# Optimization experiments

Measured on AMD Instinct MI355X. Metric: run time of the kernel, lower is better.

The kernel has to match this reference:

```python
import jax, jax.numpy as jnp
import numpy as np

B, C_IN, L = 256, 4, 2048
HNODE, GLEN = 256, 24
SIGMA_CONV, SIGMA_NEU = 0.1, 0.1
DROPPROB = 0.5


def setup_inputs() -> dict:
    key = jax.random.key(0)
    ks = jax.random.split(key, 7)
    x = jax.random.normal(ks[0], (B, C_IN, L), dtype=jnp.float32)
    wConv = SIGMA_CONV * jax.random.normal(ks[1], (HNODE, C_IN, GLEN), dtype=jnp.float32)
    wRect = -jax.random.normal(ks[2], (HNODE,), dtype=jnp.float32)
    wHidden = 0.3 * jax.random.normal(ks[3], (2 * HNODE, 2 * HNODE), dtype=jnp.float32)
    wHiddenBias = 0.3 * jax.random.normal(ks[4], (2 * HNODE,), dtype=jnp.float32)
    wNeu = SIGMA_NEU * jax.random.normal(ks[5], (2 * HNODE, 1), dtype=jnp.float32)
    wNeuBias = SIGMA_NEU * jax.random.normal(ks[6], (1,), dtype=jnp.float32)
    return {"x": x, "wConv": wConv, "wRect": wRect, "wHidden": wHidden,
            "wHiddenBias": wHiddenBias, "wNeu": wNeu, "wNeuBias": wNeuBias}


def reference(x, wConv, wRect, wHidden, wHiddenBias, wNeu, wNeuBias):
    # conv1d, stride 1, no padding: [B, HNODE, L-GLEN+1]
    conv = jax.lax.conv_general_dilated(
        x, wConv, window_strides=(1,), padding='VALID',
        dimension_numbers=('NCH', 'OIH', 'NCH'))
    rect = jnp.maximum(conv + wRect[None, :, None], 0.0)  # bias + relu-clamp
    maxPool = jnp.max(rect, axis=2)   # [B, HNODE]
    avgPool = jnp.mean(rect, axis=2)  # [B, HNODE]
    pool = jnp.concatenate([maxPool, avgPool], axis=1)  # [B, 2*HNODE]
    hid = jnp.maximum(pool @ wHidden + wHiddenBias, 0.0)
    out = DROPPROB * (hid @ wNeu) + wNeuBias  # [B, 1]
    return out
```

## Files before the change

kernel.cpp:

```cpp
#include <hip/hip_runtime.h>
#include <stdint.h>

#define CIN   4
#define LEN   2048
#define HN    256
#define GL    24
#define LOUT  2025
#define XP    2080

typedef short  s16x8 __attribute__((ext_vector_type(8)));
typedef float  f32x4 __attribute__((ext_vector_type(4)));

static __device__ __forceinline__ uint16_t f2bf(float f) {
    union { float f; uint32_t u; } v; v.f = f;
    uint32_t u = v.u;
    return (uint16_t)((u + 0x7FFFu + ((u >> 16) & 1u)) >> 16);
}

#define MKFRAG(dd, p) \
    ({ uint32_t f0_, f1_, f2_, f3_; \
       if (((p) & 1) == 0) { \
           f0_ = dd[(p)/2];   f1_ = dd[(p)/2+1]; \
           f2_ = dd[(p)/2+2]; f3_ = dd[(p)/2+3]; \
       } else { \
           f0_ = __builtin_amdgcn_alignbit(dd[((p)+1)/2],   dd[((p)-1)/2],   16); \
           f1_ = __builtin_amdgcn_alignbit(dd[((p)+1)/2+1], dd[((p)-1)/2+1], 16); \
           f2_ = __builtin_amdgcn_alignbit(dd[((p)+1)/2+2], dd[((p)-1)/2+2], 16); \
           f3_ = __builtin_amdgcn_alignbit(dd[((p)+1)/2+3], dd[((p)-1)/2+3], 16); \
       } \
       uint4 fu_ = {f0_, f1_, f2_, f3_}; __builtin_bit_cast(s16x8, fu_); })

__global__ __launch_bounds__(1024, 4) void conv_pool_kernel(
    const float* __restrict__ x, const float* __restrict__ wConv,
    const float* __restrict__ wRect, float* __restrict__ pool)
{
    __shared__ uint16_t xs[CIN * XP];
    __shared__ float pmax_l[2][HN];
    __shared__ float psum_l[2][HN];

    const int tid  = threadIdx.x;
    const int b    = blockIdx.x;
    const int lane = tid & 63;
    const int wid  = tid >> 6;
    const int wp   = wid & 7;
    const int wh   = wid >> 3;
    const int n    = lane & 15;
    const int q    = lane >> 4;

    const float* xb = x + (size_t)b * (CIN * LEN);
    #pragma unroll
    for (int it = 0; it < 2; ++it) {
        int i = (tid + it * 1024) * 4;
        float4 v = *(const float4*)(xb + i);
        int c = i >> 11, off = i & 2047;
        uint64_t pk =  (uint64_t)f2bf(v.x)
                    | ((uint64_t)f2bf(v.y) << 16)
                    | ((uint64_t)f2bf(v.z) << 32)
                    | ((uint64_t)f2bf(v.w) << 48);
        *(uint64_t*)&xs[c * XP + off] = pk;
    }
    if (tid < 64) {
        int c = tid >> 4, o = (tid & 15) * 2;
        *(uint32_t*)&xs[c * XP + 2048 + o] = 0u;
    }

    s16x8 bfrag[2][3];
    float negb[2];
    #pragma unroll
    for (int s = 0; s < 2; ++s) {
        int h = wp * 32 + s * 16 + n;
        negb[s] = -wRect[h];
        #pragma unroll
        for (int ks = 0; ks < 3; ++ks) {
            int jb = ks * 4 + q;
            const float* wp_ = wConv + h * (CIN * GL) + jb * 8;
            float4 w0 = *(const float4*)(wp_);
            float4 w1 = *(const float4*)(wp_ + 4);
            s16x8 f;
            f[0]=(short)f2bf(w0.x); f[1]=(short)f2bf(w0.y);
            f[2]=(short)f2bf(w0.z); f[3]=(short)f2bf(w0.w);
            f[4]=(short)f2bf(w1.x); f[5]=(short)f2bf(w1.y);
            f[6]=(short)f2bf(w1.z); f[7]=(short)f2bf(w1.w);
            bfrag[s][ks] = f;
        }
    }

    int abase[3];
    #pragma unroll
    for (int ks = 0; ks < 3; ++ks) {
        int jb = ks * 4 + q;
        int c = jb / 3, g0 = (jb % 3) * 8;
        abase[ks] = c * XP + g0 + 8 * n;
    }

    __syncthreads();

    float rawmax[2] = {-1e30f, -1e30f};
    float sums[2]   = {0.f, 0.f};
    const f32x4 fzero = {0.f, 0.f, 0.f, 0.f};

    #pragma unroll 1
    for (int jj = 0; jj < 8; ++jj) {
        const int j = wh * 8 + jj;
        const bool tail = (j == 15);

        uint32_t d0[8], d1[8], d2[8];
        {
            const uint4 r0 = *(const uint4*)&xs[abase[0] + 128 * j];
            const uint4 r1 = *(const uint4*)&xs[abase[0] + 128 * j + 8];
            d0[0]=r0.x; d0[1]=r0.y; d0[2]=r0.z; d0[3]=r0.w;
            d0[4]=r1.x; d0[5]=r1.y; d0[6]=r1.z; d0[7]=r1.w;
        }
        {
            const uint4 r0 = *(const uint4*)&xs[abase[1] + 128 * j];
            const uint4 r1 = *(const uint4*)&xs[abase[1] + 128 * j + 8];
            d1[0]=r0.x; d1[1]=r0.y; d1[2]=r0.z; d1[3]=r0.w;
            d1[4]=r1.x; d1[5]=r1.y; d1[6]=r1.z; d1[7]=r1.w;
        }
        {
            const uint4 r0 = *(const uint4*)&xs[abase[2] + 128 * j];
            const uint4 r1 = *(const uint4*)&xs[abase[2] + 128 * j + 8];
            d2[0]=r0.x; d2[1]=r0.y; d2[2]=r0.z; d2[3]=r0.w;
            d2[4]=r1.x; d2[5]=r1.y; d2[6]=r1.z; d2[7]=r1.w;
        }

        #pragma unroll
        for (int p = 0; p < 8; ++p) {
            s16x8 a0 = MKFRAG(d0, p);
            s16x8 a1 = MKFRAG(d1, p);
            s16x8 a2 = MKFRAG(d2, p);
            f32x4 acc[2];
            acc[0] = __builtin_amdgcn_mfma_f32_16x16x32_bf16(a0, bfrag[0][0], fzero, 0, 0, 0);
            acc[1] = __builtin_amdgcn_mfma_f32_16x16x32_bf16(a0, bfrag[1][0], fzero, 0, 0, 0);
            acc[0] = __builtin_amdgcn_mfma_f32_16x16x32_bf16(a1, bfrag[0][1], acc[0], 0, 0, 0);
            acc[1] = __builtin_amdgcn_mfma_f32_16x16x32_bf16(a1, bfrag[1][1], acc[1], 0, 0, 0);
            acc[0] = __builtin_amdgcn_mfma_f32_16x16x32_bf16(a2, bfrag[0][2], acc[0], 0, 0, 0);
            acc[1] = __builtin_amdgcn_mfma_f32_16x16x32_bf16(a2, bfrag[1][2], acc[1], 0, 0, 0);

            if (!tail) {
                #pragma unroll
                for (int s = 0; s < 2; ++s) {
                    const f32x4 a = acc[s];
                    float t0 = fmaxf(a[0], negb[s]), t1 = fmaxf(a[1], negb[s]);
                    float t2 = fmaxf(a[2], negb[s]), t3 = fmaxf(a[3], negb[s]);
                    sums[s] += (t0 + t1) + (t2 + t3);
                    rawmax[s] = fmaxf(fmaxf(rawmax[s], a[0]), a[1]);
                    rawmax[s] = fmaxf(fmaxf(rawmax[s], a[2]), a[3]);
                }
            } else {
                #pragma unroll
                for (int s = 0; s < 2; ++s) {
                    const f32x4 a = acc[s];
                    #pragma unroll
                    for (int r = 0; r < 4; ++r) {
                        int tpos = p + 128 * 15 + 32 * q + 8 * r;
                        float t = (tpos < LOUT) ? fmaxf(a[r], negb[s])
                                                : negb[s];
                        sums[s]   += t;
                        rawmax[s]  = fmaxf(rawmax[s], t);
                    }
                }
            }
        }
    }

    #pragma unroll
    for (int s = 0; s < 2; ++s) {
        float m  = rawmax[s], sm = sums[s];
        m  = fmaxf(m, __shfl_xor(m, 16, 64));  sm += __shfl_xor(sm, 16, 64);
        m  = fmaxf(m, __shfl_xor(m, 32, 64));  sm += __shfl_xor(sm, 32, 64);
        if (q == 0) {
            int h = wp * 32 + s * 16 + n;
            pmax_l[wh][h] = m;
            psum_l[wh][h] = sm;
        }
    }
    __syncthreads();

    if (tid < HN) {
        float m   = fmaxf(pmax_l[0][tid], pmax_l[1][tid]);
        float sm  = psum_l[0][tid] + psum_l[1][tid];
        float bia = wRect[tid];
        pool[(size_t)b * 512 + tid]       = fmaxf(m + bia, 0.f);
        pool[(size_t)b * 512 + 256 + tid] = (sm + 2048.f * bia) * (1.0f / 2025.0f);
    }
}

__global__ __launch_bounds__(256, 4) void mlp_kernel(
    const float* __restrict__ pool, const float* __restrict__ wH,
    const float* __restrict__ bH, const float* __restrict__ wNeu,
    const float* __restrict__ wNeuB, float* __restrict__ out)
{
    __shared__ float pl[8][512];

    const int tid = threadIdx.x;
    const int og  = blockIdx.x & 7;
    const int bg  = blockIdx.x >> 3;
    const int o   = og * 64 + (tid & 63);
    const int wv  = tid >> 6;

    const float* ps = pool + (size_t)bg * 8 * 512;
    #pragma unroll
    for (int it = 0; it < 4; ++it) {
        int i = (tid + it * 256) * 4;
        *(float4*)&pl[0][i] = *(const float4*)(ps + i);
    }
    __syncthreads();

    float acc0 = 0.f, acc1 = 0.f;
    const float* prow0 = &pl[wv * 2][0];
    const float* prow1 = &pl[wv * 2 + 1][0];
    #pragma unroll 4
    for (int i = 0; i < 512; i += 4) {
        float4 p0 = *(const float4*)(prow0 + i);
        float4 p1 = *(const float4*)(prow1 + i);
        float w0 = wH[(i + 0) * 512 + o];
        float w1 = wH[(i + 1) * 512 + o];
        float w2 = wH[(i + 2) * 512 + o];
        float w3 = wH[(i + 3) * 512 + o];
        acc0 = fmaf(p0.x, w0, acc0); acc0 = fmaf(p0.y, w1, acc0);
        acc0 = fmaf(p0.z, w2, acc0); acc0 = fmaf(p0.w, w3, acc0);
        acc1 = fmaf(p1.x, w0, acc1); acc1 = fmaf(p1.y, w1, acc1);
        acc1 = fmaf(p1.z, w2, acc1); acc1 = fmaf(p1.w, w3, acc1);
    }
    float hb  = bH[o];
    float wn  = wNeu[o];
    float v0  = fmaxf(acc0 + hb, 0.f) * wn;
    float v1  = fmaxf(acc1 + hb, 0.f) * wn;
    #pragma unroll
    for (int dlt = 1; dlt < 64; dlt <<= 1) {
        v0 += __shfl_xor(v0, dlt, 64);
        v1 += __shfl_xor(v1, dlt, 64);
    }
    if ((tid & 63) == 0) {
        int b0 = bg * 8 + wv * 2;
        float bias = (og == 0) ? wNeuB[0] : 0.f;
        atomicAdd(&out[b0],     0.5f * v0 + bias);
        atomicAdd(&out[b0 + 1], 0.5f * v1 + bias);
    }
}

extern "C" void kernel_launch(void* const* d_in, const int* in_sizes, int n_in,
                              void* d_out, int out_size, void* d_ws, size_t ws_size,
                              hipStream_t stream) {
    const float* x        = (const float*)d_in[0];
    const float* wConv    = (const float*)d_in[1];
    const float* wRect    = (const float*)d_in[2];
    const float* wHidden  = (const float*)d_in[3];
    const float* wHidBias = (const float*)d_in[4];
    const float* wNeu     = (const float*)d_in[5];
    const float* wNeuBias = (const float*)d_in[6];
    float* out  = (float*)d_out;
    float* pool = (float*)d_ws;

    hipMemsetAsync(d_out, 0, 256 * sizeof(float), stream);
    conv_pool_kernel<<<256, 1024, 0, stream>>>(x, wConv, wRect, pool);
    mlp_kernel<<<256, 256, 0, stream>>>(pool, wHidden, wHidBias, wNeu, wNeuBias, out);
}
```

Baseline: 125.4 us.

## Split conv over two blocks per sample and merge pool partials in MLP

Each sample's sequence is now split across two blocks of the conv kernel, giving 512 blocks in place of 256 so all compute units get work. Each block loads only its half of the input plus a halo, with smaller shared memory. Partial max and sum values go to a global buffer, and the bias, relu and mean finalisation moves into the MLP kernel's load phase. This adds duplicated weight-fragment setup and halo loads per block, plus an extra partial-buffer read in the MLP.

```diff
diff --git a/kernel.cpp b/kernel.cpp
--- a/kernel.cpp
+++ b/kernel.cpp
@@ -6,10 +6,12 @@
 #define HN    256
 #define GL    24
 #define LOUT  2025
-#define XP    2080
+#define XPH   1056
 
 typedef short  s16x8 __attribute__((ext_vector_type(8)));
 typedef float  f32x4 __attribute__((ext_vector_type(4)));
+
+__device__ float g_part[256][2][512];
 
 static __device__ __forceinline__ uint16_t f2bf(float f) {
     union { float f; uint32_t u; } v; v.f = f;
@@ -30,38 +32,38 @@
        } \
        uint4 fu_ = {f0_, f1_, f2_, f3_}; __builtin_bit_cast(s16x8, fu_); })
 
-__global__ __launch_bounds__(1024, 4) void conv_pool_kernel(
+__global__ __launch_bounds__(1024, 8) void conv_pool_kernel(
     const float* __restrict__ x, const float* __restrict__ wConv,
-    const float* __restrict__ wRect, float* __restrict__ pool)
+    const float* __restrict__ wRect)
 {
-    __shared__ uint16_t xs[CIN * XP];
+    __shared__ uint16_t xs[CIN * XPH];
     __shared__ float pmax_l[2][HN];
     __shared__ float psum_l[2][HN];
 
     const int tid  = threadIdx.x;
-    const int b    = blockIdx.x;
+    const int b    = blockIdx.x >> 1;
+    const int wh   = blockIdx.x & 1;
     const int lane = tid & 63;
     const int wid  = tid >> 6;
     const int wp   = wid & 7;
-    const int wh   = wid >> 3;
+    const int wq   = wid >> 3;
     const int n    = lane & 15;
     const int q    = lane >> 4;
 
     const float* xb = x + (size_t)b * (CIN * LEN);
-    #pragma unroll
-    for (int it = 0; it < 2; ++it) {
-        int i = (tid + it * 1024) * 4;
-        float4 v = *(const float4*)(xb + i);
-        int c = i >> 11, off = i & 2047;
-        uint64_t pk =  (uint64_t)f2bf(v.x)
-                    | ((uint64_t)f2bf(v.y) << 16)
-                    | ((uint64_t)f2bf(v.z) << 32)
-                    | ((uint64_t)f2bf(v.w) << 48);
-        *(uint64_t*)&xs[c * XP + off] = pk;
-    }
-    if (tid < 64) {
-        int c = tid >> 4, o = (tid & 15) * 2;
-        *(uint32_t*)&xs[c * XP + 2048 + o] = 0u;
+    for (int f = tid; f < CIN * (XPH / 4); f += 1024) {
+        int c = f / (XPH / 4);
+        int k4 = (f - c * (XPH / 4)) * 4;
+        int p0 = wh * 1024 + k4;
+        uint64_t pk = 0;
+        if (p0 < LEN) {
+            float4 v = *(const float4*)(xb + c * LEN + p0);
+            pk =  (uint64_t)f2bf(v.x)
+               | ((uint64_t)f2bf(v.y) << 16)
+               | ((uint64_t)f2bf(v.z) << 32)
+               | ((uint64_t)f2bf(v.w) << 48);
+        }
+        *(uint64_t*)&xs[c * XPH + k4] = pk;
     }
 
     s16x8 bfrag[2][3];
@@ -90,7 +92,7 @@
     for (int ks = 0; ks < 3; ++ks) {
         int jb = ks * 4 + q;
         int c = jb / 3, g0 = (jb % 3) * 8;
-        abase[ks] = c * XP + g0 + 8 * n;
+        abase[ks] = c * XPH + g0 + 8 * n;
     }
 
     __syncthreads();
@@ -100,26 +102,26 @@
     const f32x4 fzero = {0.f, 0.f, 0.f, 0.f};
 
     #pragma unroll 1
-    for (int jj = 0; jj < 8; ++jj) {
-        const int j = wh * 8 + jj;
-        const bool tail = (j == 15);
+    for (int tt = 0; tt < 4; ++tt) {
+        const int jl = wq * 4 + tt;
+        const bool tail = (wh == 1) && (jl == 7);
 
         uint32_t d0[8], d1[8], d2[8];
         {
-            const uint4 r0 = *(const uint4*)&xs[abase[0] + 128 * j];
-            const uint4 r1 = *(const uint4*)&xs[abase[0] + 128 * j + 8];
+            const uint4 r0 = *(const uint4*)&xs[abase[0] + 128 * jl];
+            const uint4 r1 = *(const uint4*)&xs[abase[0] + 128 * jl + 8];
             d0[0]=r0.x; d0[1]=r0.y; d0[2]=r0.z; d0[3]=r0.w;
             d0[4]=r1.x; d0[5]=r1.y; d0[6]=r1.z; d0[7]=r1.w;
         }
         {
-            const uint4 r0 = *(const uint4*)&xs[abase[1] + 128 * j];
-            const uint4 r1 = *(const uint4*)&xs[abase[1] + 128 * j + 8];
+            const uint4 r0 = *(const uint4*)&xs[abase[1] + 128 * jl];
+            const uint4 r1 = *(const uint4*)&xs[abase[1] + 128 * jl + 8];
             d1[0]=r0.x; d1[1]=r0.y; d1[2]=r0.z; d1[3]=r0.w;
             d1[4]=r1.x; d1[5]=r1.y; d1[6]=r1.z; d1[7]=r1.w;
         }
         {
-            const uint4 r0 = *(const uint4*)&xs[abase[2] + 128 * j];
-            const uint4 r1 = *(const uint4*)&xs[abase[2] + 128 * j + 8];
+            const uint4 r0 = *(const uint4*)&xs[abase[2] + 128 * jl];
+            const uint4 r1 = *(const uint4*)&xs[abase[2] + 128 * jl + 8];
             d2[0]=r0.x; d2[1]=r0.y; d2[2]=r0.z; d2[3]=r0.w;
             d2[4]=r1.x; d2[5]=r1.y; d2[6]=r1.z; d2[7]=r1.w;
         }
@@ -171,23 +173,20 @@
         m  = fmaxf(m, __shfl_xor(m, 32, 64));  sm += __shfl_xor(sm, 32, 64);
         if (q == 0) {
             int h = wp * 32 + s * 16 + n;
-            pmax_l[wh][h] = m;
-            psum_l[wh][h] = sm;
+            pmax_l[wq][h] = m;
+            psum_l[wq][h] = sm;
         }
     }
     __syncthreads();
 
     if (tid < HN) {
-        float m   = fmaxf(pmax_l[0][tid], pmax_l[1][tid]);
-        float sm  = psum_l[0][tid] + psum_l[1][tid];
-        float bia = wRect[tid];
-        pool[(size_t)b * 512 + tid]       = fmaxf(m + bia, 0.f);
-        pool[(size_t)b * 512 + 256 + tid] = (sm + 2048.f * bia) * (1.0f / 2025.0f);
+        g_part[b][wh][tid]       = fmaxf(pmax_l[0][tid], pmax_l[1][tid]);
+        g_part[b][wh][256 + tid] = psum_l[0][tid] + psum_l[1][tid];
     }
 }
 
 __global__ __launch_bounds__(256, 4) void mlp_kernel(
-    const float* __restrict__ pool, const float* __restrict__ wH,
+    const float* __restrict__ wRect, const float* __restrict__ wH,
     const float* __restrict__ bH, const float* __restrict__ wNeu,
     const float* __restrict__ wNeuB, float* __restrict__ out)
 {
@@ -199,11 +198,30 @@
     const int o   = og * 64 + (tid & 63);
     const int wv  = tid >> 6;
 
-    const float* ps = pool + (size_t)bg * 8 * 512;
     #pragma unroll
     for (int it = 0; it < 4; ++it) {
-        int i = (tid + it * 256) * 4;
-        *(float4*)&pl[0][i] = *(const float4*)(ps + i);
+        int i   = (tid + it * 256) * 4;
+        int smp = i >> 9;
+        int c   = i & 511;
+        const float* p0 = &g_part[bg * 8 + smp][0][c];
+        const float* p1 = &g_part[bg * 8 + smp][1][c];
+        float4 v0 = *(const float4*)p0;
+        float4 v1 = *(const float4*)p1;
+        float4 r;
+        if (c < 256) {
+            float4 wr = *(const float4*)(wRect + c);
+            r.x = fmaxf(fmaxf(v0.x, v1.x) + wr.x, 0.f);
+            r.y = fmaxf(fmaxf(v0.y, v1.y) + wr.y, 0.f);
+            r.z = fmaxf(fmaxf(v0.z, v1.z) + wr.z, 0.f);
+            r.w = fmaxf(fmaxf(v0.w, v1.w) + wr.w, 0.f);
+        } else {
+            float4 wr = *(const float4*)(wRect + c - 256);
+            r.x = (v0.x + v1.x + 2048.f * wr.x) * (1.0f / 2025.0f);
+            r.y = (v0.y + v1.y + 2048.f * wr.y) * (1.0f / 2025.0f);
+            r.z = (v0.z + v1.z + 2048.f * wr.z) * (1.0f / 2025.0f);
+            r.w = (v0.w + v1.w + 2048.f * wr.w) * (1.0f / 2025.0f);
+        }
+        *(float4*)&pl[0][i] = r;
     }
     __syncthreads();
 
@@ -251,9 +269,9 @@
     const float* wNeu     = (const float*)d_in[5];
     const float* wNeuBias = (const float*)d_in[6];
     float* out  = (float*)d_out;
-    float* pool = (float*)d_ws;
+    (void)d_ws; (void)ws_size;
 
     hipMemsetAsync(d_out, 0, 256 * sizeof(float), stream);
-    conv_pool_kernel<<<256, 1024, 0, stream>>>(x, wConv, wRect, pool);
-    mlp_kernel<<<256, 256, 0, stream>>>(pool, wHidden, wHidBias, wNeu, wNeuBias, out);
-}
+    conv_pool_kernel<<<512, 1024, 0, stream>>>(x, wConv, wRect);
+    mlp_kernel<<<256, 256, 0, stream>>>(wRect, wHidden, wHidBias, wNeu, wNeuBias, out);
+}
```

New measurement: 338.3 us. 2.7x slower.

## Halve conv block size, widen per-wave channel tile, double-buffer LDS window loads

Applied to the files above, without the earlier changes.

The conv kernel moves from 1024 to 512 threads per block, and each wave now covers 64 output channels instead of 32. This lets every A fragment built from the input window feed four MFMA chains instead of two, so fewer LDS reads and alignbit fragment builds are needed per MFMA. The time loop is software-pipelined with two register buffers, so the next window's LDS load overlaps the current MFMA work. The pool workspace also moves to a device-global array. The cost is higher register pressure (twice the B fragments and accumulators), only 16 waves per block, and a waves_per_eu hint that limits occupancy.

```diff
diff --git a/kernel.cpp b/kernel.cpp
--- a/kernel.cpp
+++ b/kernel.cpp
@@ -10,6 +10,8 @@
 
 typedef short  s16x8 __attribute__((ext_vector_type(8)));
 typedef float  f32x4 __attribute__((ext_vector_type(4)));
+
+__device__ float g_pool[256 * 512];
 
 static __device__ __forceinline__ uint16_t f2bf(float f) {
     union { float f; uint32_t u; } v; v.f = f;
@@ -30,9 +32,71 @@
        } \
        uint4 fu_ = {f0_, f1_, f2_, f3_}; __builtin_bit_cast(s16x8, fu_); })
 
-__global__ __launch_bounds__(1024, 4) void conv_pool_kernel(
+static __device__ __forceinline__ void loadW(
+    uint32_t (&D)[3][8], const uint16_t* xs, const int (&abase)[3], int j)
+{
+    #pragma unroll
+    for (int ks = 0; ks < 3; ++ks) {
+        const uint4 r0 = *(const uint4*)&xs[abase[ks] + 128 * j];
+        const uint4 r1 = *(const uint4*)&xs[abase[ks] + 128 * j + 8];
+        D[ks][0] = r0.x; D[ks][1] = r0.y; D[ks][2] = r0.z; D[ks][3] = r0.w;
+        D[ks][4] = r1.x; D[ks][5] = r1.y; D[ks][6] = r1.z; D[ks][7] = r1.w;
+    }
+}
+
+static __device__ __forceinline__ void procW(
+    const uint32_t (&D)[3][8], const s16x8 (&bfrag)[4][3],
+    const float (&negb)[4], bool tail, int q,
+    float (&rawmax)[4], float (&sums)[4])
+{
+    const f32x4 fzero = {0.f, 0.f, 0.f, 0.f};
+    #pragma unroll
+    for (int p = 0; p < 8; ++p) {
+        s16x8 a0 = MKFRAG(D[0], p);
+        s16x8 a1 = MKFRAG(D[1], p);
+        s16x8 a2 = MKFRAG(D[2], p);
+        f32x4 acc[4];
+        #pragma unroll
+        for (int s = 0; s < 4; ++s)
+            acc[s] = __builtin_amdgcn_mfma_f32_16x16x32_bf16(a0, bfrag[s][0], fzero, 0, 0, 0);
+        #pragma unroll
+        for (int s = 0; s < 4; ++s)
+            acc[s] = __builtin_amdgcn_mfma_f32_16x16x32_bf16(a1, bfrag[s][1], acc[s], 0, 0, 0);
+        #pragma unroll
+        for (int s = 0; s < 4; ++s)
+            acc[s] = __builtin_amdgcn_mfma_f32_16x16x32_bf16(a2, bfrag[s][2], acc[s], 0, 0, 0);
+
+        if (!tail) {
+            #pragma unroll
+            for (int s = 0; s < 4; ++s) {
+                const f32x4 a = acc[s];
+                float t0 = fmaxf(a[0], negb[s]), t1 = fmaxf(a[1], negb[s]);
+                float t2 = fmaxf(a[2], negb[s]), t3 = fmaxf(a[3], negb[s]);
+                sums[s] += (t0 + t1) + (t2 + t3);
+                rawmax[s] = fmaxf(fmaxf(rawmax[s], a[0]), a[1]);
+                rawmax[s] = fmaxf(fmaxf(rawmax[s], a[2]), a[3]);
+            }
+        } else {
+            #pragma unroll
+            for (int s = 0; s < 4; ++s) {
+                const f32x4 a = acc[s];
+                #pragma unroll
+                for (int r = 0; r < 4; ++r) {
+                    int tpos = p + 128 * 15 + 32 * q + 8 * r;
+                    float t = (tpos < LOUT) ? fmaxf(a[r], negb[s])
+                                            : negb[s];
+                    sums[s]   += t;
+                    rawmax[s]  = fmaxf(rawmax[s], t);
+                }
+            }
+        }
+    }
+}
+
+__global__ __launch_bounds__(512) __attribute__((amdgpu_waves_per_eu(2, 2)))
+void conv_pool_kernel(
     const float* __restrict__ x, const float* __restrict__ wConv,
-    const float* __restrict__ wRect, float* __restrict__ pool)
+    const float* __restrict__ wRect)
 {
     __shared__ uint16_t xs[CIN * XP];
     __shared__ float pmax_l[2][HN];
@@ -42,15 +106,15 @@
     const int b    = blockIdx.x;
     const int lane = tid & 63;
     const int wid  = tid >> 6;
-    const int wp   = wid & 7;
-    const int wh   = wid >> 3;
+    const int ng   = wid & 3;
+    const int jh   = wid >> 2;
     const int n    = lane & 15;
     const int q    = lane >> 4;
 
     const float* xb = x + (size_t)b * (CIN * LEN);
     #pragma unroll
-    for (int it = 0; it < 2; ++it) {
-        int i = (tid + it * 1024) * 4;
+    for (int it = 0; it < 4; ++it) {
+        int i = (tid + it * 512) * 4;
         float4 v = *(const float4*)(xb + i);
         int c = i >> 11, off = i & 2047;
         uint64_t pk =  (uint64_t)f2bf(v.x)
@@ -64,11 +128,11 @@
         *(uint32_t*)&xs[c * XP + 2048 + o] = 0u;
     }
 
-    s16x8 bfrag[2][3];
-    float negb[2];
-    #pragma unroll
-    for (int s = 0; s < 2; ++s) {
-        int h = wp * 32 + s * 16 + n;
+    s16x8 bfrag[4][3];
+    float negb[4];
+    #pragma unroll
+    for (int s = 0; s < 4; ++s) {
+        int h = ng * 64 + s * 16 + n;
         negb[s] = -wRect[h];
         #pragma unroll
         for (int ks = 0; ks < 3; ++ks) {
@@ -95,84 +159,30 @@
 
     __syncthreads();
 
-    float rawmax[2] = {-1e30f, -1e30f};
-    float sums[2]   = {0.f, 0.f};
-    const f32x4 fzero = {0.f, 0.f, 0.f, 0.f};
-
+    float rawmax[4] = {-1e30f, -1e30f, -1e30f, -1e30f};
+    float sums[4]   = {0.f, 0.f, 0.f, 0.f};
+
+    const int j0 = jh * 8;
+    uint32_t dA[3][8], dB[3][8];
+    loadW(dA, xs, abase, j0);
     #pragma unroll 1
-    for (int jj = 0; jj < 8; ++jj) {
-        const int j = wh * 8 + jj;
-        const bool tail = (j == 15);
-
-        uint32_t d0[8], d1[8], d2[8];
-        {
-            const uint4 r0 = *(const uint4*)&xs[abase[0] + 128 * j];
-            const uint4 r1 = *(const uint4*)&xs[abase[0] + 128 * j + 8];
-            d0[0]=r0.x; d0[1]=r0.y; d0[2]=r0.z; d0[3]=r0.w;
-            d0[4]=r1.x; d0[5]=r1.y; d0[6]=r1.z; d0[7]=r1.w;
-        }
-        {
-            const uint4 r0 = *(const uint4*)&xs[abase[1] + 128 * j];
-            const uint4 r1 = *(const uint4*)&xs[abase[1] + 128 * j + 8];
-            d1[0]=r0.x; d1[1]=r0.y; d1[2]=r0.z; d1[3]=r0.w;
-            d1[4]=r1.x; d1[5]=r1.y; d1[6]=r1.z; d1[7]=r1.w;
-        }
-        {
-            const uint4 r0 = *(const uint4*)&xs[abase[2] + 128 * j];
-            const uint4 r1 = *(const uint4*)&xs[abase[2] + 128 * j + 8];
-            d2[0]=r0.x; d2[1]=r0.y; d2[2]=r0.z; d2[3]=r0.w;
-            d2[4]=r1.x; d2[5]=r1.y; d2[6]=r1.z; d2[7]=r1.w;
-        }
-
-        #pragma unroll
-        for (int p = 0; p < 8; ++p) {
-            s16x8 a0 = MKFRAG(d0, p);
-            s16x8 a1 = MKFRAG(d1, p);
-            s16x8 a2 = MKFRAG(d2, p);
-            f32x4 acc[2];
-            acc[0] = __builtin_amdgcn_mfma_f32_16x16x32_bf16(a0, bfrag[0][0], fzero, 0, 0, 0);
-            acc[1] = __builtin_amdgcn_mfma_f32_16x16x32_bf16(a0, bfrag[1][0], fzero, 0, 0, 0);
-            acc[0] = __builtin_amdgcn_mfma_f32_16x16x32_bf16(a1, bfrag[0][1], acc[0], 0, 0, 0);
-            acc[1] = __builtin_amdgcn_mfma_f32_16x16x32_bf16(a1, bfrag[1][1], acc[1], 0, 0, 0);
-            acc[0] = __builtin_amdgcn_mfma_f32_16x16x32_bf16(a2, bfrag[0][2], acc[0], 0, 0, 0);
-            acc[1] = __builtin_amdgcn_mfma_f32_16x16x32_bf16(a2, bfrag[1][2], acc[1], 0, 0, 0);
-
-            if (!tail) {
-                #pragma unroll
-                for (int s = 0; s < 2; ++s) {
-                    const f32x4 a = acc[s];
-                    float t0 = fmaxf(a[0], negb[s]), t1 = fmaxf(a[1], negb[s]);
-                    float t2 = fmaxf(a[2], negb[s]), t3 = fmaxf(a[3], negb[s]);
-                    sums[s] += (t0 + t1) + (t2 + t3);
-                    rawmax[s] = fmaxf(fmaxf(rawmax[s], a[0]), a[1]);
-                    rawmax[s] = fmaxf(fmaxf(rawmax[s], a[2]), a[3]);
-                }
-            } else {
-                #pragma unroll
-                for (int s = 0; s < 2; ++s) {
-                    const f32x4 a = acc[s];
-                    #pragma unroll
-                    for (int r = 0; r < 4; ++r) {
-                        int tpos = p + 128 * 15 + 32 * q + 8 * r;
-                        float t = (tpos < LOUT) ? fmaxf(a[r], negb[s])
-                                                : negb[s];
-                        sums[s]   += t;
-                        rawmax[s]  = fmaxf(rawmax[s], t);
-                    }
-                }
-            }
-        }
-    }
-
-    #pragma unroll
-    for (int s = 0; s < 2; ++s) {
+    for (int jj = 0; jj < 8; jj += 2) {
+        loadW(dB, xs, abase, j0 + jj + 1);
+        procW(dA, bfrag, negb, false, q, rawmax, sums);
+        int jn = (jj + 2 < 8) ? j0 + jj + 2 : 15;
+        loadW(dA, xs, abase, jn);
+        procW(dB, bfrag, negb, (jh == 1) && (jj == 6), q, rawmax, sums);
+    }
+
+    #pragma unroll
+    for (int s = 0; s < 4; ++s) {
         float m  = rawmax[s], sm = sums[s];
         m  = fmaxf(m, __shfl_xor(m, 16, 64));  sm += __shfl_xor(sm, 16, 64);
         m  = fmaxf(m, __shfl_xor(m, 32, 64));  sm += __shfl_xor(sm, 32, 64);
         if (q == 0) {
-            int h = wp * 32 + s * 16 + n;
-            pmax_l[wh][h] = m;
-            psum_l[wh][h] = sm;
+            int h = ng * 64 + s * 16 + n;
+            pmax_l[jh][h] = m;
+            psum_l[jh][h] = sm;
         }
     }
     __syncthreads();
@@ -181,15 +191,15 @@
         float m   = fmaxf(pmax_l[0][tid], pmax_l[1][tid]);
         float sm  = psum_l[0][tid] + psum_l[1][tid];
         float bia = wRect[tid];
-        pool[(size_t)b * 512 + tid]       = fmaxf(m + bia, 0.f);
-        pool[(size_t)b * 512 + 256 + tid] = (sm + 2048.f * bia) * (1.0f / 2025.0f);
+        g_pool[(size_t)b * 512 + tid]       = fmaxf(m + bia, 0.f);
+        g_pool[(size_t)b * 512 + 256 + tid] = (sm + 2048.f * bia) * (1.0f / 2025.0f);
     }
 }
 
 __global__ __launch_bounds__(256, 4) void mlp_kernel(
-    const float* __restrict__ pool, const float* __restrict__ wH,
-    const float* __restrict__ bH, const float* __restrict__ wNeu,
-    const float* __restrict__ wNeuB, float* __restrict__ out)
+    const float* __restrict__ wH, const float* __restrict__ bH,
+    const float* __restrict__ wNeu, const float* __restrict__ wNeuB,
+    float* __restrict__ out)
 {
     __shared__ float pl[8][512];
 
@@ -199,7 +209,7 @@
     const int o   = og * 64 + (tid & 63);
     const int wv  = tid >> 6;
 
-    const float* ps = pool + (size_t)bg * 8 * 512;
+    const float* ps = g_pool + (size_t)bg * 8 * 512;
     #pragma unroll
     for (int it = 0; it < 4; ++it) {
         int i = (tid + it * 256) * 4;
@@ -251,9 +261,9 @@
     const float* wNeu     = (const float*)d_in[5];
     const float* wNeuBias = (const float*)d_in[6];
     float* out  = (float*)d_out;
-    float* pool = (float*)d_ws;
+    (void)d_ws; (void)ws_size;
 
     hipMemsetAsync(d_out, 0, 256 * sizeof(float), stream);
-    conv_pool_kernel<<<256, 1024, 0, stream>>>(x, wConv, wRect, pool);
-    mlp_kernel<<<256, 256, 0, stream>>>(pool, wHidden, wHidBias, wNeu, wNeuBias, out);
-}
+    conv_pool_kernel<<<256, 512, 0, stream>>>(x, wConv, wRect);
+    mlp_kernel<<<256, 256, 0, stream>>>(wHidden, wHidBias, wNeu, wNeuBias, out);
+}
```

Measured after the change: 126.4 us. No clear change (+0.8%).
